# Performance work log

Hardware: AMD Instinct MI355X
Metric: run time of the kernel (lower is better)

Reference implementation:

```python
import jax, jax.numpy as jnp
import numpy as np

B, T, C = 4, 2048, 1024
NH = 16
HD = C // NH  # 64


def setup_inputs() -> dict:
    key = jax.random.key(0)
    k1, k2, k3, k4, k5 = jax.random.split(key, 5)
    s_in = 1.0 / np.sqrt(C)
    return {
        "x": jax.random.normal(k1, (B, T, C), dtype=jnp.float32),
        "attention_mask": jnp.ones((B, T), dtype=jnp.float32),
        "W_qkv": jax.random.normal(k2, (C, 3 * C), dtype=jnp.float32) * s_in,
        "b_qkv": jnp.zeros((3 * C,), dtype=jnp.float32),
        "W_out": jax.random.normal(k3, (C, C), dtype=jnp.float32) * s_in,
        "b_out": jnp.zeros((C,), dtype=jnp.float32),
    }


def reference(x, attention_mask, W_qkv, b_qkv, W_out, b_out):
    Bx, Tx, Cx = x.shape
    # QKV projection: (B,T,3C)
    qkv = x @ W_qkv + b_qkv
    Q, K, V = jnp.split(qkv, 3, axis=-1)
    # (B, NH, T, HD)
    Q = Q.reshape(Bx, Tx, NH, HD).transpose(0, 2, 1, 3)
    K = K.reshape(Bx, Tx, NH, HD).transpose(0, 2, 1, 3)
    V = V.reshape(Bx, Tx, NH, HD).transpose(0, 2, 1, 3)
    # scaled scores (B, NH, T, T)
    scores = jnp.einsum("bhqd,bhkd->bhqk", Q, K) * (1.0 / np.sqrt(HD))
    # causal mask: set strictly-upper triangle to -inf (mask-fill semantics)
    causal = jnp.tril(jnp.ones((Tx, Tx), dtype=bool))[None, None]
    scores = jnp.where(causal, scores, -jnp.inf)
    # additive padding mask
    pad = (1.0 - attention_mask)[:, None, None, :] * jnp.finfo(scores.dtype).min
    scores = scores + pad
    attn = jax.nn.softmax(scores, axis=-1)
    # weighted values -> (B, T, C)
    wv = jnp.einsum("bhqk,bhkd->bhqd", attn, V)
    wv = wv.transpose(0, 2, 1, 3).reshape(Bx, Tx, Cx)
    return wv @ W_out + b_out
```

## Files before the change

kernel.cpp:

```cpp
#include <hip/hip_runtime.h>
#include <math.h>

constexpr int BB = 4;
constexpr int TT = 2048;
constexpr int CC = 1024;
constexpr int NHH = 16;
constexpr int HDD = 64;
constexpr int C3 = 3 * CC;

typedef __bf16 bf16x8 __attribute__((ext_vector_type(8)));
typedef float  f32x4  __attribute__((ext_vector_type(4)));

__device__ __forceinline__ unsigned short f2bf(float x) {
    union { float f; unsigned u; } v; v.f = x;
    unsigned r = v.u + 0x7fffu + ((v.u >> 16) & 1u);
    return (unsigned short)(r >> 16);
}

#define AS1(p) ((const __attribute__((address_space(1))) void*)(p))
#define AS3(p) ((__attribute__((address_space(3))) void*)(p))

constexpr int CAST_BLOCKS = (BB * TT * CC / 4) / 256;
constexpr int TQKV_BLOCKS = (C3 / 64) * (CC / 64);
constexpr int TOUT_BLOCKS = (CC / 64) * (CC / 64);

__global__ __launch_bounds__(256) void prep(
    const float* __restrict__ x,
    const float* __restrict__ Wqkv,
    const float* __restrict__ Wout,
    unsigned short* __restrict__ xb,
    unsigned short* __restrict__ Wqkvt,
    unsigned short* __restrict__ Woutt)
{
    __shared__ float tile[64][65];
    const int bid = blockIdx.x;
    const int t = threadIdx.x;

    if (bid < CAST_BLOCKS) {
        const int i = bid * 256 + t;
        float4 v = ((const float4*)x)[i];
        ushort4 o;
        o.x = f2bf(v.x); o.y = f2bf(v.y); o.z = f2bf(v.z); o.w = f2bf(v.w);
        ((ushort4*)xb)[i] = o;
        return;
    }

    const float* src; unsigned short* dst; int R, Cn, r0, c0;
    if (bid < CAST_BLOCKS + TQKV_BLOCKS) {
        const int tb = bid - CAST_BLOCKS;
        src = Wqkv; dst = Wqkvt; R = CC; Cn = C3;
        c0 = (tb % (C3 / 64)) * 64; r0 = (tb / (C3 / 64)) * 64;
    } else {
        const int tb = bid - CAST_BLOCKS - TQKV_BLOCKS;
        src = Wout; dst = Woutt; R = CC; Cn = CC;
        c0 = (tb % (CC / 64)) * 64; r0 = (tb / (CC / 64)) * 64;
    }

    const int lr = t >> 4, lc = (t & 15) * 4;
    #pragma unroll
    for (int s = 0; s < 4; ++s) {
        float4 v = *(const float4*)&src[(size_t)(r0 + lr + s * 16) * Cn + c0 + lc];
        tile[lr + s * 16][lc + 0] = v.x;
        tile[lr + s * 16][lc + 1] = v.y;
        tile[lr + s * 16][lc + 2] = v.z;
        tile[lr + s * 16][lc + 3] = v.w;
    }
    __syncthreads();
    const int oi = t >> 2, oc = (t & 3) * 16;
    unsigned short buf[16];
    #pragma unroll
    for (int u = 0; u < 16; ++u)
        buf[u] = f2bf(tile[oc + u][oi]);
    unsigned short* d = &dst[(size_t)(c0 + oi) * R + r0 + oc];
    *(uint4*)(d + 0) = *(uint4*)&buf[0];
    *(uint4*)(d + 8) = *(uint4*)&buf[8];
}

template<bool BF16OUT, bool VSPLIT>
__global__ __launch_bounds__(256) void gemm_bt_mfma(
    const unsigned short* __restrict__ A,
    const unsigned short* __restrict__ Bt,
    const float* __restrict__ bias,
    void* __restrict__ OutV,
    unsigned short* __restrict__ Vt_g,
    int M, int N, int K, int scale_n, float scale)
{
    __shared__ alignas(16) unsigned short As[128 * 64];
    __shared__ alignas(16) unsigned short Bs[128 * 64];

    const int tid  = threadIdx.x;
    const int w    = tid >> 6;
    const int lane = tid & 63;
    const int quad = lane >> 4;
    const int col  = lane & 15;
    const int m0 = blockIdx.y * 128, n0 = blockIdx.x * 128;
    const int wr = w >> 1, wc = w & 1;

    f32x4 acc[4][4];
    #pragma unroll
    for (int i = 0; i < 4; ++i)
        #pragma unroll
        for (int j = 0; j < 4; ++j)
            #pragma unroll
            for (int r = 0; r < 4; ++r)
                acc[i][j][r] = 0.0f;

    const int srow = tid >> 3;
    const int spos = tid & 7;
    char* AsB = (char*)As;
    char* BsB = (char*)Bs;

    for (int k0 = 0; k0 < K; k0 += 64) {
        if (k0) __syncthreads();
        #pragma unroll
        for (int i = 0; i < 4; ++i) {
            const int row = srow + 32 * i;
            const int sch = spos ^ (row & 7);
            __builtin_amdgcn_global_load_lds(
                AS1(A + (size_t)(m0 + row) * K + k0 + sch * 8),
                AS3(AsB + i * 4096 + w * 1024), 16, 0, 0);
            __builtin_amdgcn_global_load_lds(
                AS1(Bt + (size_t)(n0 + row) * K + k0 + sch * 8),
                AS3(BsB + i * 4096 + w * 1024), 16, 0, 0);
        }
        __syncthreads();

        #pragma unroll
        for (int ks = 0; ks < 2; ++ks) {
            bf16x8 af[4], bf[4];
            #pragma unroll
            for (int i = 0; i < 4; ++i) {
                const int ra = wr * 64 + i * 16 + col;
                const int pa = ((quad + ks * 4) ^ (ra & 7)) * 8;
                af[i] = *(const bf16x8*)&As[ra * 64 + pa];
                const int rb = wc * 64 + i * 16 + col;
                const int pb = ((quad + ks * 4) ^ (rb & 7)) * 8;
                bf[i] = *(const bf16x8*)&Bs[rb * 64 + pb];
            }
            #pragma unroll
            for (int i = 0; i < 4; ++i)
                #pragma unroll
                for (int j = 0; j < 4; ++j)
                    acc[i][j] = __builtin_amdgcn_mfma_f32_16x16x32_bf16(af[i], bf[j], acc[i][j], 0, 0, 0);
        }
    }

    if (VSPLIT && n0 >= 2 * CC) {
        #pragma unroll
        for (int i = 0; i < 4; ++i) {
            const int mb   = m0 + wr * 64 + i * 16 + quad * 4;
            const int bidx = mb >> 11;
            const int tloc = mb & 2047;
            #pragma unroll
            for (int j = 0; j < 4; ++j) {
                const int n  = n0 + wc * 64 + j * 16 + col;
                const int hh = (n - 2 * CC) >> 6;
                const int dd = (n - 2 * CC) & 63;
                unsigned short pk[4];
                #pragma unroll
                for (int r = 0; r < 4; ++r)
                    pk[r] = f2bf(acc[i][j][r] + bias[n]);
                *(uint2*)&Vt_g[(((size_t)bidx * NHH + hh) * HDD + dd) * TT + tloc] =
                    *(const uint2*)pk;
            }
        }
    } else {
        #pragma unroll
        for (int i = 0; i < 4; ++i) {
            #pragma unroll
            for (int r = 0; r < 4; ++r) {
                const int m = m0 + wr * 64 + i * 16 + quad * 4 + r;
                #pragma unroll
                for (int j = 0; j < 4; ++j) {
                    const int n = n0 + wc * 64 + j * 16 + col;
                    float v = acc[i][j][r] + bias[n];
                    if (n < scale_n) v *= scale;
                    if (BF16OUT)
                        ((unsigned short*)OutV)[(size_t)m * N + n] = f2bf(v);
                    else
                        ((float*)OutV)[(size_t)m * N + n] = v;
                }
            }
        }
    }
}

constexpr int PP = 72;
constexpr float SM2 = 17.312340490667561f;

__global__ __launch_bounds__(512, 6) void attn_mfma(
    const unsigned short* __restrict__ QKV,
    const unsigned short* __restrict__ Vt_g,
    const float* __restrict__ amask,
    unsigned short* __restrict__ WV)
{
    __shared__ alignas(16) unsigned short Ks [2][64 * 64];
    __shared__ alignas(16) unsigned short Vts[2][64 * 64];
    __shared__ alignas(16) __bf16        Ps[8][16 * PP];

    const int tid  = threadIdx.x;
    const int w    = tid >> 6;
    const int lane = tid & 63;
    const int quad = lane >> 4;
    const int col  = lane & 15;
    const int bh = blockIdx.y, b = bh >> 4, h = bh & 15;
    const int jx = blockIdx.x;

    const size_t base = (size_t)b * TT * C3 + (size_t)h * HDD;
    const unsigned short* Qg = QKV + base;
    const unsigned short* Kg = QKV + base + CC;
    const unsigned short* Vt = Vt_g + (size_t)bh * HDD * TT;

    const int srow = tid >> 3;
    const int sch  = (tid & 7) ^ (srow & 7);
    const unsigned short* Ksrc = Kg + (size_t)srow * C3 + sch * 8;
    const unsigned short* Vsrc = Vt + (size_t)srow * TT + sch * 8;
    char* KsB  = (char*)&Ks[0][0];
    char* VtsB = (char*)&Vts[0][0];

    #pragma unroll
    for (int ph = 0; ph < 2; ++ph) {
        const int qb    = ph ? (15 - jx) : jx;
        const int qbase = qb * 128;
        const int qw    = qbase + w * 16;

        bf16x8 qf0 = *(const bf16x8*)(Qg + (size_t)(qw + col) * C3 + quad * 8);
        bf16x8 qf1 = *(const bf16x8*)(Qg + (size_t)(qw + col) * C3 + 32 + quad * 8);

        f32x4 o[4];
        float l[4];
        #pragma unroll
        for (int t = 0; t < 4; ++t)
            #pragma unroll
            for (int r = 0; r < 4; ++r) o[t][r] = 0.0f;
        #pragma unroll
        for (int r = 0; r < 4; ++r) l[r] = 0.0f;

        const int ntiles = (qbase >> 6) + 2;

        __builtin_amdgcn_global_load_lds(AS1(Ksrc), AS3(KsB  + w * 1024), 16, 0, 0);
        __builtin_amdgcn_global_load_lds(AS1(Vsrc), AS3(VtsB + w * 1024), 16, 0, 0);
        __syncthreads();

        for (int it = 0; it < ntiles; ++it) {
            const int kt  = it << 6;
            const int cur = it & 1;

            if (it + 1 < ntiles) {
                __builtin_amdgcn_global_load_lds(
                    AS1(Ksrc + (size_t)(kt + 64) * C3),
                    AS3(KsB + (cur ^ 1) * 8192 + w * 1024), 16, 0, 0);
                __builtin_amdgcn_global_load_lds(
                    AS1(Vsrc + (kt + 64)),
                    AS3(VtsB + (cur ^ 1) * 8192 + w * 1024), 16, 0, 0);
            }

            if (kt <= qw + 15) {
                const unsigned short* ksb = &Ks[cur][0];
                const unsigned short* vsb = &Vts[cur][0];

                f32x4 s[4];
                #pragma unroll
                for (int t = 0; t < 4; ++t) {
                    const int row = t * 16 + col;
                    const int c0 = (quad ^ (row & 7)) * 8;
                    const int c1 = ((quad + 4) ^ (row & 7)) * 8;
                    bf16x8 k0 = *(const bf16x8*)&ksb[row * 64 + c0];
                    bf16x8 k1 = *(const bf16x8*)&ksb[row * 64 + c1];
                    f32x4 z;
                    #pragma unroll
                    for (int r = 0; r < 4; ++r) z[r] = -SM2;
                    z = __builtin_amdgcn_mfma_f32_16x16x32_bf16(qf0, k0, z, 0, 0, 0);
                    z = __builtin_amdgcn_mfma_f32_16x16x32_bf16(qf1, k1, z, 0, 0, 0);
                    s[t] = z;
                }

                const bool needc = (kt + 64 > qw);
                float mval[4];
                #pragma unroll
                for (int t = 0; t < 4; ++t)
                    mval[t] = amask[b * TT + kt + t * 16 + col];
                #pragma unroll
                for (int t = 0; t < 4; ++t) {
                    const int key = kt + t * 16 + col;
                    #pragma unroll
                    for (int r = 0; r < 4; ++r) {
                        float p = exp2f(s[t][r]) * mval[t];
                        if (needc && key > qw + quad * 4 + r) p = 0.0f;
                        l[r] += p;
                        Ps[w][(quad * 4 + r) * PP + t * 16 + col] = (__bf16)p;
                    }
                }

                bf16x8 p0 = *(const bf16x8*)&Ps[w][col * PP + quad * 8];
                bf16x8 p1 = *(const bf16x8*)&Ps[w][col * PP + 32 + quad * 8];
                #pragma unroll
                for (int t = 0; t < 4; ++t) {
                    const int row = t * 16 + col;
                    const int c0 = (quad ^ (row & 7)) * 8;
                    const int c1 = ((quad + 4) ^ (row & 7)) * 8;
                    bf16x8 v0 = *(const bf16x8*)&vsb[row * 64 + c0];
                    bf16x8 v1 = *(const bf16x8*)&vsb[row * 64 + c1];
                    o[t] = __builtin_amdgcn_mfma_f32_16x16x32_bf16(p0, v0, o[t], 0, 0, 0);
                    o[t] = __builtin_amdgcn_mfma_f32_16x16x32_bf16(p1, v1, o[t], 0, 0, 0);
                }
            }
            __syncthreads();
        }

        #pragma unroll
        for (int off = 1; off < 16; off <<= 1)
            #pragma unroll
            for (int r = 0; r < 4; ++r)
                l[r] += __shfl_xor(l[r], off);
        #pragma unroll
        for (int r = 0; r < 4; ++r) {
            const float inv = 1.0f / l[r];
            const int q = qw + quad * 4 + r;
            unsigned short* dst = WV + ((size_t)b * TT + q) * CC + (size_t)h * HDD;
            #pragma unroll
            for (int t = 0; t < 4; ++t)
                dst[t * 16 + col] = f2bf(o[t][r] * inv);
        }
    }
}

extern "C" void kernel_launch(void* const* d_in, const int* in_sizes, int n_in,
                              void* d_out, int out_size, void* d_ws, size_t ws_size,
                              hipStream_t stream) {
    const float* x     = (const float*)d_in[0];
    const float* amask = (const float*)d_in[1];
    const float* Wqkv  = (const float*)d_in[2];
    const float* bqkv  = (const float*)d_in[3];
    const float* Wout  = (const float*)d_in[4];
    const float* bout  = (const float*)d_in[5];
    float* out = (float*)d_out;

    const int M = BB * TT;

    unsigned short* xb    = (unsigned short*)d_ws;
    unsigned short* Wqkvt = xb    + (size_t)M * CC;
    unsigned short* Woutt = Wqkvt + (size_t)C3 * CC;
    unsigned short* qkv   = Woutt + (size_t)CC * CC;
    unsigned short* wvb   = qkv   + (size_t)M * C3;
    unsigned short* Vt_g  = wvb   + (size_t)M * CC;

    dim3 blk(256);

    prep<<<dim3(CAST_BLOCKS + TQKV_BLOCKS + TOUT_BLOCKS), blk, 0, stream>>>(
        x, Wqkv, Wout, xb, Wqkvt, Woutt);

    gemm_bt_mfma<true, true><<<dim3(C3 / 128, M / 128), blk, 0, stream>>>(
        xb, Wqkvt, bqkv, qkv, Vt_g, M, C3, CC, CC, 0.18033688011112043f);
    attn_mfma<<<dim3(TT / 256, BB * NHH), dim3(512), 0, stream>>>(qkv, Vt_g, amask, wvb);
    gemm_bt_mfma<false, false><<<dim3(CC / 128, M / 128), blk, 0, stream>>>(
        wvb, Woutt, bout, out, nullptr, M, CC, CC, 0, 1.0f);
}
```

Before: 272.8 us.

## Give each attention wave two 16-row query groups with 256-thread blocks

The attention kernel now runs 4 waves of 256 threads instead of 8 waves of 512. Each wave handles 32 query rows as two 16-row groups, so every K/V fragment read from LDS feeds twice as many MFMAs, and each thread issues two global-to-LDS loads per tile. It also swaps exp2f for the hardware exp2 builtin. The aim is fewer LDS reads per MFMA, at the cost of more registers per wave and fewer waves per block to hide latency.

```diff
diff --git a/kernel.cpp b/kernel.cpp
--- a/kernel.cpp
+++ b/kernel.cpp
@@ -188,7 +188,7 @@
 constexpr int PP = 72;
 constexpr float SM2 = 17.312340490667561f;
 
-__global__ __launch_bounds__(512, 6) void attn_mfma(
+__global__ __launch_bounds__(256, 3) void attn_mfma(
     const unsigned short* __restrict__ QKV,
     const unsigned short* __restrict__ Vt_g,
     const float* __restrict__ amask,
@@ -196,7 +196,7 @@
 {
     __shared__ alignas(16) unsigned short Ks [2][64 * 64];
     __shared__ alignas(16) unsigned short Vts[2][64 * 64];
-    __shared__ alignas(16) __bf16        Ps[8][16 * PP];
+    __shared__ alignas(16) __bf16        Ps[4][32 * PP];
 
     const int tid  = threadIdx.x;
     const int w    = tid >> 6;
@@ -212,9 +212,7 @@
     const unsigned short* Vt = Vt_g + (size_t)bh * HDD * TT;
 
     const int srow = tid >> 3;
-    const int sch  = (tid & 7) ^ (srow & 7);
-    const unsigned short* Ksrc = Kg + (size_t)srow * C3 + sch * 8;
-    const unsigned short* Vsrc = Vt + (size_t)srow * TT + sch * 8;
+    const int spos = tid & 7;
     char* KsB  = (char*)&Ks[0][0];
     char* VtsB = (char*)&Vts[0][0];
 
@@ -222,24 +220,41 @@
     for (int ph = 0; ph < 2; ++ph) {
         const int qb    = ph ? (15 - jx) : jx;
         const int qbase = qb * 128;
-        const int qw    = qbase + w * 16;
-
-        bf16x8 qf0 = *(const bf16x8*)(Qg + (size_t)(qw + col) * C3 + quad * 8);
-        bf16x8 qf1 = *(const bf16x8*)(Qg + (size_t)(qw + col) * C3 + 32 + quad * 8);
-
-        f32x4 o[4];
-        float l[4];
-        #pragma unroll
-        for (int t = 0; t < 4; ++t)
-            #pragma unroll
-            for (int r = 0; r < 4; ++r) o[t][r] = 0.0f;
-        #pragma unroll
-        for (int r = 0; r < 4; ++r) l[r] = 0.0f;
-
-        const int ntiles = (qbase >> 6) + 2;
-
-        __builtin_amdgcn_global_load_lds(AS1(Ksrc), AS3(KsB  + w * 1024), 16, 0, 0);
-        __builtin_amdgcn_global_load_lds(AS1(Vsrc), AS3(VtsB + w * 1024), 16, 0, 0);
+        const int qw    = qbase + w * 32;
+
+        bf16x8 qf[2][2];
+        #pragma unroll
+        for (int rg = 0; rg < 2; ++rg)
+            #pragma unroll
+            for (int hf = 0; hf < 2; ++hf)
+                qf[rg][hf] = *(const bf16x8*)(Qg +
+                    (size_t)(qw + rg * 16 + col) * C3 + hf * 32 + quad * 8);
+
+        f32x4 o[2][4];
+        float l[2][4];
+        #pragma unroll
+        for (int rg = 0; rg < 2; ++rg) {
+            #pragma unroll
+            for (int t = 0; t < 4; ++t)
+                #pragma unroll
+                for (int r = 0; r < 4; ++r) o[rg][t][r] = 0.0f;
+            #pragma unroll
+            for (int r = 0; r < 4; ++r) l[rg][r] = 0.0f;
+        }
+
+        const int ntiles = 2 * qb + 2;
+
+        #pragma unroll
+        for (int i = 0; i < 2; ++i) {
+            const int row = srow + 32 * i;
+            const int sch = spos ^ (row & 7);
+            __builtin_amdgcn_global_load_lds(
+                AS1(Kg + (size_t)row * C3 + sch * 8),
+                AS3(KsB + i * 4096 + w * 1024), 16, 0, 0);
+            __builtin_amdgcn_global_load_lds(
+                AS1(Vt + (size_t)row * TT + sch * 8),
+                AS3(VtsB + i * 4096 + w * 1024), 16, 0, 0);
+        }
         __syncthreads();
 
         for (int it = 0; it < ntiles; ++it) {
@@ -247,80 +262,95 @@
             const int cur = it & 1;
 
             if (it + 1 < ntiles) {
-                __builtin_amdgcn_global_load_lds(
-                    AS1(Ksrc + (size_t)(kt + 64) * C3),
-                    AS3(KsB + (cur ^ 1) * 8192 + w * 1024), 16, 0, 0);
-                __builtin_amdgcn_global_load_lds(
-                    AS1(Vsrc + (kt + 64)),
-                    AS3(VtsB + (cur ^ 1) * 8192 + w * 1024), 16, 0, 0);
-            }
-
-            if (kt <= qw + 15) {
+                #pragma unroll
+                for (int i = 0; i < 2; ++i) {
+                    const int row = srow + 32 * i;
+                    const int sch = spos ^ (row & 7);
+                    __builtin_amdgcn_global_load_lds(
+                        AS1(Kg + (size_t)(kt + 64 + row) * C3 + sch * 8),
+                        AS3(KsB + (cur ^ 1) * 8192 + i * 4096 + w * 1024), 16, 0, 0);
+                    __builtin_amdgcn_global_load_lds(
+                        AS1(Vt + (size_t)row * TT + kt + 64 + sch * 8),
+                        AS3(VtsB + (cur ^ 1) * 8192 + i * 4096 + w * 1024), 16, 0, 0);
+                }
+            }
+
+            if (kt <= qw + 31) {
                 const unsigned short* ksb = &Ks[cur][0];
                 const unsigned short* vsb = &Vts[cur][0];
 
-                f32x4 s[4];
-                #pragma unroll
-                for (int t = 0; t < 4; ++t) {
-                    const int row = t * 16 + col;
-                    const int c0 = (quad ^ (row & 7)) * 8;
-                    const int c1 = ((quad + 4) ^ (row & 7)) * 8;
-                    bf16x8 k0 = *(const bf16x8*)&ksb[row * 64 + c0];
-                    bf16x8 k1 = *(const bf16x8*)&ksb[row * 64 + c1];
-                    f32x4 z;
-                    #pragma unroll
-                    for (int r = 0; r < 4; ++r) z[r] = -SM2;
-                    z = __builtin_amdgcn_mfma_f32_16x16x32_bf16(qf0, k0, z, 0, 0, 0);
-                    z = __builtin_amdgcn_mfma_f32_16x16x32_bf16(qf1, k1, z, 0, 0, 0);
-                    s[t] = z;
-                }
-
-                const bool needc = (kt + 64 > qw);
                 float mval[4];
                 #pragma unroll
                 for (int t = 0; t < 4; ++t)
                     mval[t] = amask[b * TT + kt + t * 16 + col];
-                #pragma unroll
-                for (int t = 0; t < 4; ++t) {
-                    const int key = kt + t * 16 + col;
+
+                #pragma unroll
+                for (int rg = 0; rg < 2; ++rg) {
+                    if (kt > qw + rg * 16 + 15) continue;
+                    const int q0 = qw + rg * 16;
+
+                    f32x4 s[4];
                     #pragma unroll
-                    for (int r = 0; r < 4; ++r) {
-                        float p = exp2f(s[t][r]) * mval[t];
-                        if (needc && key > qw + quad * 4 + r) p = 0.0f;
-                        l[r] += p;
-                        Ps[w][(quad * 4 + r) * PP + t * 16 + col] = (__bf16)p;
+                    for (int t = 0; t < 4; ++t) {
+                        const int row = t * 16 + col;
+                        const int c0 = (quad ^ (row & 7)) * 8;
+                        const int c1 = ((quad + 4) ^ (row & 7)) * 8;
+                        bf16x8 k0 = *(const bf16x8*)&ksb[row * 64 + c0];
+                        bf16x8 k1 = *(const bf16x8*)&ksb[row * 64 + c1];
+                        f32x4 z;
+                        #pragma unroll
+                        for (int r = 0; r < 4; ++r) z[r] = -SM2;
+                        z = __builtin_amdgcn_mfma_f32_16x16x32_bf16(qf[rg][0], k0, z, 0, 0, 0);
+                        z = __builtin_amdgcn_mfma_f32_16x16x32_bf16(qf[rg][1], k1, z, 0, 0, 0);
+                        s[t] = z;
+                    }
+
+                    const bool needc = (kt + 64 > q0);
+                    #pragma unroll
+                    for (int t = 0; t < 4; ++t) {
+                        const int key = kt + t * 16 + col;
+                        #pragma unroll
+                        for (int r = 0; r < 4; ++r) {
+                            float p = __builtin_amdgcn_exp2f(s[t][r]) * mval[t];
+                            if (needc && key > q0 + quad * 4 + r) p = 0.0f;
+                            l[rg][r] += p;
+                            Ps[w][(rg * 16 + quad * 4 + r) * PP + t * 16 + col] = (__bf16)p;
+                        }
+                    }
+
+                    bf16x8 p0 = *(const bf16x8*)&Ps[w][(rg * 16 + col) * PP + quad * 8];
+                    bf16x8 p1 = *(const bf16x8*)&Ps[w][(rg * 16 + col) * PP + 32 + quad * 8];
+                    #pragma unroll
+                    for (int t = 0; t < 4; ++t) {
+                        const int row = t * 16 + col;
+                        const int c0 = (quad ^ (row & 7)) * 8;
+                        const int c1 = ((quad + 4) ^ (row & 7)) * 8;
+                        bf16x8 v0 = *(const bf16x8*)&vsb[row * 64 + c0];
+                        bf16x8 v1 = *(const bf16x8*)&vsb[row * 64 + c1];
+                        o[rg][t] = __builtin_amdgcn_mfma_f32_16x16x32_bf16(p0, v0, o[rg][t], 0, 0, 0);
+                        o[rg][t] = __builtin_amdgcn_mfma_f32_16x16x32_bf16(p1, v1, o[rg][t], 0, 0, 0);
                     }
                 }
-
-                bf16x8 p0 = *(const bf16x8*)&Ps[w][col * PP + quad * 8];
-                bf16x8 p1 = *(const bf16x8*)&Ps[w][col * PP + 32 + quad * 8];
-                #pragma unroll
-                for (int t = 0; t < 4; ++t) {
-                    const int row = t * 16 + col;
-                    const int c0 = (quad ^ (row & 7)) * 8;
-                    const int c1 = ((quad + 4) ^ (row & 7)) * 8;
-                    bf16x8 v0 = *(const bf16x8*)&vsb[row * 64 + c0];
-                    bf16x8 v1 = *(const bf16x8*)&vsb[row * 64 + c1];
-                    o[t] = __builtin_amdgcn_mfma_f32_16x16x32_bf16(p0, v0, o[t], 0, 0, 0);
-                    o[t] = __builtin_amdgcn_mfma_f32_16x16x32_bf16(p1, v1, o[t], 0, 0, 0);
-                }
             }
             __syncthreads();
         }
 
         #pragma unroll
-        for (int off = 1; off < 16; off <<= 1)
-            #pragma unroll
-            for (int r = 0; r < 4; ++r)
-                l[r] += __shfl_xor(l[r], off);
-        #pragma unroll
-        for (int r = 0; r < 4; ++r) {
-            const float inv = 1.0f / l[r];
-            const int q = qw + quad * 4 + r;
-            unsigned short* dst = WV + ((size_t)b * TT + q) * CC + (size_t)h * HDD;
-            #pragma unroll
-            for (int t = 0; t < 4; ++t)
-                dst[t * 16 + col] = f2bf(o[t][r] * inv);
+        for (int rg = 0; rg < 2; ++rg) {
+            #pragma unroll
+            for (int off = 1; off < 16; off <<= 1)
+                #pragma unroll
+                for (int r = 0; r < 4; ++r)
+                    l[rg][r] += __shfl_xor(l[rg][r], off);
+            #pragma unroll
+            for (int r = 0; r < 4; ++r) {
+                const float inv = 1.0f / l[rg][r];
+                const int q = qw + rg * 16 + quad * 4 + r;
+                unsigned short* dst = WV + ((size_t)b * TT + q) * CC + (size_t)h * HDD;
+                #pragma unroll
+                for (int t = 0; t < 4; ++t)
+                    dst[t * 16 + col] = f2bf(o[rg][t][r] * inv);
+            }
         }
     }
 }
@@ -352,7 +382,7 @@
 
     gemm_bt_mfma<true, true><<<dim3(C3 / 128, M / 128), blk, 0, stream>>>(
         xb, Wqkvt, bqkv, qkv, Vt_g, M, C3, CC, CC, 0.18033688011112043f);
-    attn_mfma<<<dim3(TT / 256, BB * NHH), dim3(512), 0, stream>>>(qkv, Vt_g, amask, wvb);
+    attn_mfma<<<dim3(TT / 256, BB * NHH), blk, 0, stream>>>(qkv, Vt_g, amask, wvb);
     gemm_bt_mfma<false, false><<<dim3(CC / 128, M / 128), blk, 0, stream>>>(
         wvb, Woutt, bout, out, nullptr, M, CC, CC, 0, 1.0f);
 }
```

Measured after the change: 267.3 us. 1.02x faster.

## Split QKV into head-contiguous K and tiled Vt, fold padding mask into score bias

Applied to the files above, without the earlier changes.

The QKV GEMM epilogue now writes Q, a per-head contiguous K layout, and V transposed into 64x64 key tiles, so the attention kernel's async K/V tile loads read contiguous memory instead of rows strided by 3C. The padding mask is precomputed in the prep kernel as an additive bias (combined with the softmax offset) that seeds the MFMA accumulator, replacing a per-element multiply. exp2f is replaced by the hardware exp2 intrinsic. The cost is scattered 2-byte stores in the K epilogue and one more small workspace buffer.

```diff
diff --git a/kernel.cpp b/kernel.cpp
--- a/kernel.cpp
+++ b/kernel.cpp
@@ -20,17 +20,22 @@
 #define AS1(p) ((const __attribute__((address_space(1))) void*)(p))
 #define AS3(p) ((__attribute__((address_space(3))) void*)(p))
 
+constexpr float SM2 = 17.312340490667561f;
+
 constexpr int CAST_BLOCKS = (BB * TT * CC / 4) / 256;
 constexpr int TQKV_BLOCKS = (C3 / 64) * (CC / 64);
 constexpr int TOUT_BLOCKS = (CC / 64) * (CC / 64);
+constexpr int KB_BLOCKS   = (BB * TT) / 256;
 
 __global__ __launch_bounds__(256) void prep(
     const float* __restrict__ x,
     const float* __restrict__ Wqkv,
     const float* __restrict__ Wout,
+    const float* __restrict__ amask,
     unsigned short* __restrict__ xb,
     unsigned short* __restrict__ Wqkvt,
-    unsigned short* __restrict__ Woutt)
+    unsigned short* __restrict__ Woutt,
+    float* __restrict__ kbias)
 {
     __shared__ float tile[64][65];
     const int bid = blockIdx.x;
@@ -42,6 +47,11 @@
         ushort4 o;
         o.x = f2bf(v.x); o.y = f2bf(v.y); o.z = f2bf(v.z); o.w = f2bf(v.w);
         ((ushort4*)xb)[i] = o;
+        return;
+    }
+    if (bid >= CAST_BLOCKS + TQKV_BLOCKS + TOUT_BLOCKS) {
+        const int i = (bid - CAST_BLOCKS - TQKV_BLOCKS - TOUT_BLOCKS) * 256 + t;
+        kbias[i] = (amask[i] - 1.0f) * 1.0e38f - SM2;
         return;
     }
 
@@ -76,14 +86,16 @@
     *(uint4*)(d + 8) = *(uint4*)&buf[8];
 }
 
-template<bool BF16OUT, bool VSPLIT>
+template<bool VSPLIT>
 __global__ __launch_bounds__(256) void gemm_bt_mfma(
     const unsigned short* __restrict__ A,
     const unsigned short* __restrict__ Bt,
     const float* __restrict__ bias,
-    void* __restrict__ OutV,
-    unsigned short* __restrict__ Vt_g,
-    int M, int N, int K, int scale_n, float scale)
+    float* __restrict__ OutF,
+    unsigned short* __restrict__ Qp,
+    unsigned short* __restrict__ Kp,
+    unsigned short* __restrict__ Vtp,
+    int M, int N, int K, float qscale)
 {
     __shared__ alignas(16) unsigned short As[128 * 64];
     __shared__ alignas(16) unsigned short Bs[128 * 64];
@@ -145,53 +157,79 @@
         }
     }
 
-    if (VSPLIT && n0 >= 2 * CC) {
-        #pragma unroll
-        for (int i = 0; i < 4; ++i) {
-            const int mb   = m0 + wr * 64 + i * 16 + quad * 4;
-            const int bidx = mb >> 11;
-            const int tloc = mb & 2047;
-            #pragma unroll
-            for (int j = 0; j < 4; ++j) {
-                const int n  = n0 + wc * 64 + j * 16 + col;
-                const int hh = (n - 2 * CC) >> 6;
-                const int dd = (n - 2 * CC) & 63;
-                unsigned short pk[4];
-                #pragma unroll
-                for (int r = 0; r < 4; ++r)
-                    pk[r] = f2bf(acc[i][j][r] + bias[n]);
-                *(uint2*)&Vt_g[(((size_t)bidx * NHH + hh) * HDD + dd) * TT + tloc] =
-                    *(const uint2*)pk;
+    if (VSPLIT) {
+        if (n0 < CC) {
+            #pragma unroll
+            for (int i = 0; i < 4; ++i)
+                #pragma unroll
+                for (int r = 0; r < 4; ++r) {
+                    const int m = m0 + wr * 64 + i * 16 + quad * 4 + r;
+                    #pragma unroll
+                    for (int j = 0; j < 4; ++j) {
+                        const int n = n0 + wc * 64 + j * 16 + col;
+                        Qp[(size_t)m * CC + n] = f2bf((acc[i][j][r] + bias[n]) * qscale);
+                    }
+                }
+        } else if (n0 < 2 * CC) {
+            #pragma unroll
+            for (int i = 0; i < 4; ++i) {
+                const int mb   = m0 + wr * 64 + i * 16 + quad * 4;
+                const int bidx = mb >> 11;
+                const int tloc = mb & 2047;
+                #pragma unroll
+                for (int j = 0; j < 4; ++j) {
+                    const int n  = n0 + wc * 64 + j * 16 + col;
+                    const int hh = (n - CC) >> 6;
+                    const int dd = (n - CC) & 63;
+                    #pragma unroll
+                    for (int r = 0; r < 4; ++r)
+                        Kp[(((size_t)bidx * NHH + hh) * TT + tloc + r) * HDD + dd] =
+                            f2bf(acc[i][j][r] + bias[n]);
+                }
+            }
+        } else {
+            #pragma unroll
+            for (int i = 0; i < 4; ++i) {
+                const int mb   = m0 + wr * 64 + i * 16 + quad * 4;
+                const int bidx = mb >> 11;
+                const int tloc = mb & 2047;
+                const int ktile = tloc >> 6, tc = tloc & 63;
+                #pragma unroll
+                for (int j = 0; j < 4; ++j) {
+                    const int n  = n0 + wc * 64 + j * 16 + col;
+                    const int hh = (n - 2 * CC) >> 6;
+                    const int dd = (n - 2 * CC) & 63;
+                    unsigned short pk[4];
+                    #pragma unroll
+                    for (int r = 0; r < 4; ++r)
+                        pk[r] = f2bf(acc[i][j][r] + bias[n]);
+                    *(uint2*)&Vtp[((((size_t)bidx * NHH + hh) * 32 + ktile) * HDD + dd) * 64 + tc] =
+                        *(const uint2*)pk;
+                }
             }
         }
     } else {
         #pragma unroll
-        for (int i = 0; i < 4; ++i) {
+        for (int i = 0; i < 4; ++i)
             #pragma unroll
             for (int r = 0; r < 4; ++r) {
                 const int m = m0 + wr * 64 + i * 16 + quad * 4 + r;
                 #pragma unroll
                 for (int j = 0; j < 4; ++j) {
                     const int n = n0 + wc * 64 + j * 16 + col;
-                    float v = acc[i][j][r] + bias[n];
-                    if (n < scale_n) v *= scale;
-                    if (BF16OUT)
-                        ((unsigned short*)OutV)[(size_t)m * N + n] = f2bf(v);
-                    else
-                        ((float*)OutV)[(size_t)m * N + n] = v;
-                }
-            }
-        }
+                    OutF[(size_t)m * N + n] = acc[i][j][r] + bias[n];
+                }
+            }
     }
 }
 
 constexpr int PP = 72;
-constexpr float SM2 = 17.312340490667561f;
 
 __global__ __launch_bounds__(512, 6) void attn_mfma(
-    const unsigned short* __restrict__ QKV,
-    const unsigned short* __restrict__ Vt_g,
-    const float* __restrict__ amask,
+    const unsigned short* __restrict__ Qp,
+    const unsigned short* __restrict__ Kp,
+    const unsigned short* __restrict__ Vtp,
+    const float* __restrict__ kbias,
     unsigned short* __restrict__ WV)
 {
     __shared__ alignas(16) unsigned short Ks [2][64 * 64];
@@ -206,15 +244,13 @@
     const int bh = blockIdx.y, b = bh >> 4, h = bh & 15;
     const int jx = blockIdx.x;
 
-    const size_t base = (size_t)b * TT * C3 + (size_t)h * HDD;
-    const unsigned short* Qg = QKV + base;
-    const unsigned short* Kg = QKV + base + CC;
-    const unsigned short* Vt = Vt_g + (size_t)bh * HDD * TT;
+    const unsigned short* Qg = Qp + (size_t)b * TT * CC + (size_t)h * HDD;
+    const unsigned short* Kg = Kp + (size_t)bh * TT * HDD;
+    const unsigned short* Vg = Vtp + (size_t)bh * 32 * HDD * 64;
+    const float* kb_g = kbias + b * TT;
 
     const int srow = tid >> 3;
     const int sch  = (tid & 7) ^ (srow & 7);
-    const unsigned short* Ksrc = Kg + (size_t)srow * C3 + sch * 8;
-    const unsigned short* Vsrc = Vt + (size_t)srow * TT + sch * 8;
     char* KsB  = (char*)&Ks[0][0];
     char* VtsB = (char*)&Vts[0][0];
 
@@ -224,8 +260,8 @@
         const int qbase = qb * 128;
         const int qw    = qbase + w * 16;
 
-        bf16x8 qf0 = *(const bf16x8*)(Qg + (size_t)(qw + col) * C3 + quad * 8);
-        bf16x8 qf1 = *(const bf16x8*)(Qg + (size_t)(qw + col) * C3 + 32 + quad * 8);
+        bf16x8 qf0 = *(const bf16x8*)(Qg + (size_t)(qw + col) * CC + quad * 8);
+        bf16x8 qf1 = *(const bf16x8*)(Qg + (size_t)(qw + col) * CC + 32 + quad * 8);
 
         f32x4 o[4];
         float l[4];
@@ -236,10 +272,12 @@
         #pragma unroll
         for (int r = 0; r < 4; ++r) l[r] = 0.0f;
 
-        const int ntiles = (qbase >> 6) + 2;
-
-        __builtin_amdgcn_global_load_lds(AS1(Ksrc), AS3(KsB  + w * 1024), 16, 0, 0);
-        __builtin_amdgcn_global_load_lds(AS1(Vsrc), AS3(VtsB + w * 1024), 16, 0, 0);
+        const int ntiles = 2 * qb + 2;
+
+        __builtin_amdgcn_global_load_lds(
+            AS1(Kg + (size_t)srow * HDD + sch * 8), AS3(KsB + w * 1024), 16, 0, 0);
+        __builtin_amdgcn_global_load_lds(
+            AS1(Vg + (size_t)srow * 64 + sch * 8), AS3(VtsB + w * 1024), 16, 0, 0);
         __syncthreads();
 
         for (int it = 0; it < ntiles; ++it) {
@@ -248,16 +286,21 @@
 
             if (it + 1 < ntiles) {
                 __builtin_amdgcn_global_load_lds(
-                    AS1(Ksrc + (size_t)(kt + 64) * C3),
+                    AS1(Kg + (size_t)(kt + 64 + srow) * HDD + sch * 8),
                     AS3(KsB + (cur ^ 1) * 8192 + w * 1024), 16, 0, 0);
                 __builtin_amdgcn_global_load_lds(
-                    AS1(Vsrc + (kt + 64)),
+                    AS1(Vg + ((size_t)(it + 1) * 64 + srow) * 64 + sch * 8),
                     AS3(VtsB + (cur ^ 1) * 8192 + w * 1024), 16, 0, 0);
             }
 
             if (kt <= qw + 15) {
                 const unsigned short* ksb = &Ks[cur][0];
                 const unsigned short* vsb = &Vts[cur][0];
+
+                float kb[4];
+                #pragma unroll
+                for (int t = 0; t < 4; ++t)
+                    kb[t] = kb_g[kt + t * 16 + col];
 
                 f32x4 s[4];
                 #pragma unroll
@@ -269,23 +312,19 @@
                     bf16x8 k1 = *(const bf16x8*)&ksb[row * 64 + c1];
                     f32x4 z;
                     #pragma unroll
-                    for (int r = 0; r < 4; ++r) z[r] = -SM2;
+                    for (int r = 0; r < 4; ++r) z[r] = kb[t];
                     z = __builtin_amdgcn_mfma_f32_16x16x32_bf16(qf0, k0, z, 0, 0, 0);
                     z = __builtin_amdgcn_mfma_f32_16x16x32_bf16(qf1, k1, z, 0, 0, 0);
                     s[t] = z;
                 }
 
                 const bool needc = (kt + 64 > qw);
-                float mval[4];
-                #pragma unroll
-                for (int t = 0; t < 4; ++t)
-                    mval[t] = amask[b * TT + kt + t * 16 + col];
                 #pragma unroll
                 for (int t = 0; t < 4; ++t) {
                     const int key = kt + t * 16 + col;
                     #pragma unroll
                     for (int r = 0; r < 4; ++r) {
-                        float p = exp2f(s[t][r]) * mval[t];
+                        float p = __builtin_amdgcn_exp2f(s[t][r]);
                         if (needc && key > qw + quad * 4 + r) p = 0.0f;
                         l[r] += p;
                         Ps[w][(quad * 4 + r) * PP + t * 16 + col] = (__bf16)p;
@@ -341,18 +380,21 @@
     unsigned short* xb    = (unsigned short*)d_ws;
     unsigned short* Wqkvt = xb    + (size_t)M * CC;
     unsigned short* Woutt = Wqkvt + (size_t)C3 * CC;
-    unsigned short* qkv   = Woutt + (size_t)CC * CC;
-    unsigned short* wvb   = qkv   + (size_t)M * C3;
-    unsigned short* Vt_g  = wvb   + (size_t)M * CC;
+    unsigned short* Qp    = Woutt + (size_t)CC * CC;
+    unsigned short* Kp    = Qp    + (size_t)M * CC;
+    unsigned short* Vtp   = Kp    + (size_t)M * CC;
+    unsigned short* wvb   = Vtp   + (size_t)M * CC;
+    float*          kbias = (float*)(wvb + (size_t)M * CC);
 
     dim3 blk(256);
 
-    prep<<<dim3(CAST_BLOCKS + TQKV_BLOCKS + TOUT_BLOCKS), blk, 0, stream>>>(
-        x, Wqkv, Wout, xb, Wqkvt, Woutt);
-
-    gemm_bt_mfma<true, true><<<dim3(C3 / 128, M / 128), blk, 0, stream>>>(
-        xb, Wqkvt, bqkv, qkv, Vt_g, M, C3, CC, CC, 0.18033688011112043f);
-    attn_mfma<<<dim3(TT / 256, BB * NHH), dim3(512), 0, stream>>>(qkv, Vt_g, amask, wvb);
-    gemm_bt_mfma<false, false><<<dim3(CC / 128, M / 128), blk, 0, stream>>>(
-        wvb, Woutt, bout, out, nullptr, M, CC, CC, 0, 1.0f);
+    prep<<<dim3(CAST_BLOCKS + TQKV_BLOCKS + TOUT_BLOCKS + KB_BLOCKS), blk, 0, stream>>>(
+        x, Wqkv, Wout, amask, xb, Wqkvt, Woutt, kbias);
+
+    gemm_bt_mfma<true><<<dim3(C3 / 128, M / 128), blk, 0, stream>>>(
+        xb, Wqkvt, bqkv, nullptr, Qp, Kp, Vtp, M, C3, CC, 0.18033688011112043f);
+    attn_mfma<<<dim3(TT / 256, BB * NHH), dim3(512), 0, stream>>>(
+        Qp, Kp, Vtp, kbias, wvb);
+    gemm_bt_mfma<false><<<dim3(CC / 128, M / 128), blk, 0, stream>>>(
+        wvb, Woutt, bout, out, nullptr, nullptr, nullptr, M, CC, CC, 1.0f);
 }
```

New measurement: 257.4 us. 1.06x faster.
